# Kernel optimization log

Measured on AMD Instinct MI355X. Metric: run time of the kernel, lower is better.

Reference implementation:

```python
import jax, jax.numpy as jnp
import numpy as np

N = 100000          # nodes
E = 3200000         # edges
C_IN = 64
HIDDEN = 64
NUM_CLASSES = 10
NUM_GRAPHS = 256
EPS = 1e-5


def _graph_conv(x, src, dst, w_rel, w_root, b):
    # PyG GraphConv(aggr='mean'): out_i = W_rel * mean_{j->i} x_j + W_root * x_i + b
    msg_sum = jax.ops.segment_sum(x[src], dst, num_segments=N)            # [N, C]
    cnt = jax.ops.segment_sum(jnp.ones((src.shape[0], 1), x.dtype), dst,
                              num_segments=N)                             # [N, 1]
    agg = msg_sum / jnp.maximum(cnt, 1.0)
    return agg @ w_rel + x @ w_root + b


def _batch_norm(x, gamma, beta):
    # PyG BatchNorm in training mode: batch stats over the node dimension
    mean = jnp.mean(x, axis=0)
    var = jnp.var(x, axis=0)
    return (x - mean) * jax.lax.rsqrt(var + EPS) * gamma + beta


def setup_inputs() -> dict:
    key = jax.random.key(0)
    ks = jax.random.split(key, 20)
    x = jax.random.normal(ks[0], (N, C_IN), dtype=jnp.float32)
    edge_index = jax.random.randint(ks[1], (2, E), 0, N, dtype=jnp.int32)
    batch = jnp.sort(jax.random.randint(ks[2], (N,), 0, NUM_GRAPHS, dtype=jnp.int32))

    def lin(k, fan_in, fan_out):
        s = 1.0 / np.sqrt(fan_in)
        return jax.random.uniform(k, (fan_in, fan_out), jnp.float32, -s, s)

    dims = [(C_IN, 16), (16, 32), (32, 32), (32, HIDDEN)]
    params = {}
    ki = 3
    for i, (ci, co) in enumerate(dims, start=1):
        params[f"w_rel{i}"] = lin(ks[ki], ci, co); ki += 1
        params[f"w_root{i}"] = lin(ks[ki], ci, co); ki += 1
        params[f"b{i}"] = jnp.zeros((co,), jnp.float32)
        params[f"g{i}"] = jnp.ones((co,), jnp.float32)
        params[f"be{i}"] = jnp.zeros((co,), jnp.float32)
    params["w_lin1"] = lin(ks[ki], HIDDEN, HIDDEN); ki += 1
    params["b_lin1"] = jnp.zeros((HIDDEN,), jnp.float32)
    params["w_lin2"] = lin(ks[ki], HIDDEN, NUM_CLASSES); ki += 1
    params["b_lin2"] = jnp.zeros((NUM_CLASSES,), jnp.float32)

    return {"x": x, "edge_index": edge_index, "batch": batch, **params}


def reference(x, edge_index, batch,
              w_rel1, w_root1, b1, g1, be1,
              w_rel2, w_root2, b2, g2, be2,
              w_rel3, w_root3, b3, g3, be3,
              w_rel4, w_root4, b4, g4, be4,
              w_lin1, b_lin1, w_lin2, b_lin2):
    src, dst = edge_index[0], edge_index[1]
    h = jax.nn.elu(_batch_norm(_graph_conv(x, src, dst, w_rel1, w_root1, b1), g1, be1))
    h = jax.nn.elu(_batch_norm(_graph_conv(h, src, dst, w_rel2, w_root2, b2), g2, be2))
    h = jax.nn.elu(_batch_norm(_graph_conv(h, src, dst, w_rel3, w_root3, b3), g3, be3))
    h = jax.nn.elu(_batch_norm(_graph_conv(h, src, dst, w_rel4, w_root4, b4), g4, be4))
    # global mean pool over graphs
    pooled = jax.ops.segment_sum(h, batch, num_segments=NUM_GRAPHS)
    cnt = jax.ops.segment_sum(jnp.ones((N, 1), h.dtype), batch, num_segments=NUM_GRAPHS)
    pooled = pooled / jnp.maximum(cnt, 1.0)
    z = jax.nn.relu(pooled @ w_lin1 + b_lin1)
    # dropout omitted (deterministic / eval mode)
    logits = z @ w_lin2 + b_lin2
    return jax.nn.log_softmax(logits, axis=-1)
```

## Files before the change

kernel.cpp:

```cpp
#include <hip/hip_runtime.h>
#include <hip/hip_bf16.h>
#include <math.h>

#define NGRAPHS 256
#define BSHIFT 8
#define NBUCK 512
#define NSORT 256
#define LGRID 1024
#define GCHUNK 1024
#define SMASK 0x00FFFFFFu

__device__ __forceinline__ float bf2f(unsigned short u) {
    return __uint_as_float((unsigned)u << 16);
}
__device__ __forceinline__ unsigned short f2bf(float f) {
    unsigned u = __float_as_uint(f);
    unsigned r = (u + 0x7FFFu + ((u >> 16) & 1u)) >> 16;
    return (unsigned short)r;
}

__global__ __launch_bounds__(256) void k_bhist(const int* __restrict__ dst, int* __restrict__ hmat, int E,
                                               const float* __restrict__ x, const float* __restrict__ w_rel1,
                                               unsigned short* __restrict__ y1b,
                                               int* __restrict__ colpos, int N) {
    int bid = blockIdx.x, tid = threadIdx.x;
    if (bid < NSORT) {
        __shared__ int hist[NBUCK];
        for (int i = tid; i < NBUCK; i += 256) hist[i] = 0;
        __syncthreads();
        int chunk = (E + NSORT - 1) / NSORT;
        int lo = bid * chunk;
        int hi = lo + chunk; if (hi > E) hi = E;
        for (int i = lo + tid; i < hi; i += 256)
            atomicAdd(&hist[__builtin_nontemporal_load(dst + i) >> BSHIFT], 1);
        __syncthreads();
        for (int i = tid; i < NBUCK; i += 256) {
            int h = hist[i];
            int base = atomicAdd(&colpos[i], h);
            hmat[(size_t)bid * NBUCK + i] = base;
        }
    } else {
        __shared__ float s_rel[64 * 16];
        for (int i = tid; i < 64 * 16; i += 256) s_rel[i] = w_rel1[i];
        __syncthreads();
        int total = N * 4;
        int nb = gridDim.x - NSORT;
        for (int i = (bid - NSORT) * 256 + tid; i < total; i += nb * 256) {
            int n = i >> 2, c0 = (i & 3) << 2;
            const float4* mp = (const float4*)(x + (size_t)n * 64);
            float4 acc; acc.x = 0.f; acc.y = 0.f; acc.z = 0.f; acc.w = 0.f;
#pragma unroll
            for (int k2 = 0; k2 < 16; k2++) {
                float4 v = mp[k2];
                const float* wr = &s_rel[(k2 * 4) * 16 + c0];
                float4 w0 = *(const float4*)(wr);
                float4 w1 = *(const float4*)(wr + 16);
                float4 w2 = *(const float4*)(wr + 32);
                float4 w3 = *(const float4*)(wr + 48);
                acc.x += v.x * w0.x + v.y * w1.x + v.z * w2.x + v.w * w3.x;
                acc.y += v.x * w0.y + v.y * w1.y + v.z * w2.y + v.w * w3.y;
                acc.z += v.x * w0.z + v.y * w1.z + v.z * w2.z + v.w * w3.z;
                acc.w += v.x * w0.w + v.y * w1.w + v.z * w2.w + v.w * w3.w;
            }
            ushort4 o; o.x = f2bf(acc.x); o.y = f2bf(acc.y); o.z = f2bf(acc.z); o.w = f2bf(acc.w);
            *(ushort4*)(y1b + (size_t)n * 16 + c0) = o;
        }
    }
}

__global__ __launch_bounds__(512) void k_bscatter(const int* __restrict__ src, const int* __restrict__ dst,
                                                  const int* __restrict__ hmat, const int* __restrict__ colpos,
                                                  int* __restrict__ bstart_g,
                                                  unsigned* __restrict__ ebuf, int E) {
    __shared__ int s[NBUCK];
    __shared__ int cur[NBUCK];
    int tid = threadIdx.x;
    int b = blockIdx.x;
    int v = colpos[tid];
    s[tid] = v;
    __syncthreads();
    for (int off = 1; off < NBUCK; off <<= 1) {
        int t = (tid >= off) ? s[tid - off] : 0;
        __syncthreads();
        s[tid] += t;
        __syncthreads();
    }
    int excl = s[tid] - v;
    if (b == 0) {
        bstart_g[tid] = excl;
        if (tid == NBUCK - 1) bstart_g[NBUCK] = s[NBUCK - 1];
    }
    cur[tid] = excl + hmat[(size_t)b * NBUCK + tid];
    __syncthreads();
    int chunk = (E + NSORT - 1) / NSORT;
    int lo = b * chunk;
    int hi = lo + chunk; if (hi > E) hi = E;
    for (int i = lo + tid; i < hi; i += 512) {
        int d = __builtin_nontemporal_load(dst + i);
        int sv = __builtin_nontemporal_load(src + i);
        int p = atomicAdd(&cur[d >> BSHIFT], 1);
        ebuf[p] = (unsigned)sv | ((unsigned)(d & 255) << 24);
    }
}

__global__ __launch_bounds__(256) void k_sort2(const unsigned* __restrict__ ebuf, const int* __restrict__ bstart,
                                               int* __restrict__ csr, int* __restrict__ row_start, int N) {
    __shared__ int hist[256];
    __shared__ int sc[256];
    __shared__ int scur[256];
    int b = blockIdx.x;
    int e0 = bstart[b], e1 = bstart[b + 1];
    hist[threadIdx.x] = 0;
    __syncthreads();
    for (int i = e0 + threadIdx.x; i < e1; i += 256)
        atomicAdd(&hist[__builtin_nontemporal_load(ebuf + i) >> 24], 1);
    __syncthreads();
    sc[threadIdx.x] = hist[threadIdx.x];
    __syncthreads();
    for (int off = 1; off < 256; off <<= 1) {
        int t = (threadIdx.x >= off) ? sc[threadIdx.x - off] : 0;
        __syncthreads();
        sc[threadIdx.x] += t;
        __syncthreads();
    }
    {
        int inc = sc[threadIdx.x];
        int ex = inc - hist[threadIdx.x];
        scur[threadIdx.x] = e0 + ex;
        int node = (b << BSHIFT) + threadIdx.x;
        if (node < N) row_start[node] = e0 + ex;
        if (node == N - 1) row_start[N] = e0 + inc;
    }
    __syncthreads();
    for (int i = e0 + threadIdx.x; i < e1; i += 256) {
        unsigned w = __builtin_nontemporal_load(ebuf + i);
        int p = atomicAdd(&scur[w >> 24], 1);
        csr[p] = (int)(w & SMASK);
    }
}

template <int C>
__global__ __launch_bounds__(256) void k_gather(const unsigned short* __restrict__ h,
                                                const int* __restrict__ row_start,
                                                const int* __restrict__ csr, float* __restrict__ agg, int N) {
    constexpr int LPR = C / 4;
    constexpr int EPP = 64 / LPR;
    constexpr int BATCH = 4 * EPP;
    __shared__ int sbuf[GCHUNK];
    int lane = threadIdx.x & 63;
    int w = threadIdx.x >> 6;
    int nb = blockIdx.x * 4;
    int wid = nb + w;
    bool act = wid < N;
    int nb_end = nb + 4; if (nb_end > N) nb_end = N;
    int eb0 = row_start[nb];
    int eb1 = row_start[nb_end];
    int r0 = act ? row_start[wid] : 0;
    int r1 = act ? row_start[wid + 1] : 0;
    int es = lane / LPR;
    int cq = (lane % LPR) * 4;

    float a0 = 0.f, a1 = 0.f, a2 = 0.f, a3 = 0.f;
    for (int base = eb0; base < eb1; base += GCHUNK) {
        int len = eb1 - base; if (len > GCHUNK) len = GCHUNK;
        __syncthreads();
        for (int i = threadIdx.x; i < len; i += 256)
            sbuf[i] = __builtin_nontemporal_load(csr + base + i);
        __syncthreads();
        if (act) {
            int lo = (r0 > base ? r0 : base) - base;
            int hiv = r1 < base + len ? r1 : base + len;
            int hi = hiv - base;
            for (int j0 = lo; j0 < hi; j0 += BATCH) {
                int s[4]; bool p[4];
#pragma unroll
                for (int u = 0; u < 4; u++) {
                    int j = j0 + u * EPP + es;
                    p[u] = j < hi;
                    s[u] = sbuf[p[u] ? j : j0];
                }
                ushort4 v[4];
#pragma unroll
                for (int u = 0; u < 4; u++)
                    v[u] = *(const ushort4*)(h + (size_t)s[u] * C + cq);
#pragma unroll
                for (int u = 0; u < 4; u++) {
                    if (p[u]) {
                        a0 += bf2f(v[u].x); a1 += bf2f(v[u].y);
                        a2 += bf2f(v[u].z); a3 += bf2f(v[u].w);
                    }
                }
            }
        }
    }
#pragma unroll
    for (int off = LPR; off < 64; off <<= 1) {
        a0 += __shfl_xor(a0, off, 64);
        a1 += __shfl_xor(a1, off, 64);
        a2 += __shfl_xor(a2, off, 64);
        a3 += __shfl_xor(a3, off, 64);
    }
    if (act && lane < LPR) {
        int deg = r1 - r0;
        float rec = 1.0f / (float)(deg > 0 ? deg : 1);
        float4 o; o.x = a0 * rec; o.y = a1 * rec; o.z = a2 * rec; o.w = a3 * rec;
        *(float4*)(agg + (size_t)wid * C + cq) = o;
    }
}

template <int CI, int CO, bool HAS_REL, bool ADD_AGG, bool IN_BF16>
__global__ __launch_bounds__(256) void k_lin_stats(const void* __restrict__ hroot_v, const float* __restrict__ hrel,
                                                   const float* __restrict__ w_rel, const float* __restrict__ w_root,
                                                   const float* __restrict__ bias,
                                                   float* __restrict__ out, float* __restrict__ gsl, int N) {
    constexpr int NPW = 64 / CO;
    __shared__ float part[4][2 * CO];
    int tid = threadIdx.x;
    int lane = tid & 63;
    int w = tid >> 6;
    int ch = lane % CO;
    int sub = lane / CO;

    float wro[CI];
#pragma unroll
    for (int ci = 0; ci < CI; ci++) wro[ci] = w_root[ci * CO + ch];
    float wre[HAS_REL ? CI : 1];
    if (HAS_REL) {
#pragma unroll
        for (int ci = 0; ci < CI; ci++) wre[ci] = w_rel[ci * CO + ch];
    }
    float bch = bias[ch];

    int ngrp = (N + NPW - 1) / NPW;
    int gw = blockIdx.x * 4 + w;
    int nwv = gridDim.x * 4;
    float ssum = 0.f, qsum = 0.f;
    for (int g = gw; g < ngrp; g += nwv) {
        int n = g * NPW + sub;
        if (n < N) {
            float acc = bch;
            if (ADD_AGG) acc += hrel[(size_t)n * CO + ch];
#pragma unroll
            for (int cb = 0; cb < CI / 4; cb++) {
                float f0, f1, f2, f3;
                if (IN_BF16) {
                    ushort4 v = *(const ushort4*)((const unsigned short*)hroot_v + (size_t)n * CI + cb * 4);
                    f0 = bf2f(v.x); f1 = bf2f(v.y); f2 = bf2f(v.z); f3 = bf2f(v.w);
                } else {
                    float4 v = *(const float4*)((const float*)hroot_v + (size_t)n * CI + cb * 4);
                    f0 = v.x; f1 = v.y; f2 = v.z; f3 = v.w;
                }
                acc += f0 * wro[cb * 4 + 0] + f1 * wro[cb * 4 + 1]
                     + f2 * wro[cb * 4 + 2] + f3 * wro[cb * 4 + 3];
                if (HAS_REL) {
                    float4 a = *(const float4*)(hrel + (size_t)n * CI + cb * 4);
                    acc += a.x * wre[cb * 4 + 0] + a.y * wre[cb * 4 + 1]
                         + a.z * wre[cb * 4 + 2] + a.w * wre[cb * 4 + 3];
                }
            }
            out[(size_t)n * CO + ch] = acc;
            ssum += acc; qsum += acc * acc;
        }
    }
#pragma unroll
    for (int off = CO; off < 64; off <<= 1) {
        ssum += __shfl_xor(ssum, off, 64);
        qsum += __shfl_xor(qsum, off, 64);
    }
    if (lane < CO) { part[w][lane] = ssum; part[w][CO + lane] = qsum; }
    __syncthreads();
    if (tid < 2 * CO) {
        float v = part[0][tid] + part[1][tid] + part[2][tid] + part[3][tid];
        atomicAdd(&gsl[tid], v);
    }
}

template <int CO>
__global__ __launch_bounds__(256) void k_bn_elu(const float* __restrict__ h, const float* __restrict__ gsl,
                                                const float* __restrict__ g, const float* __restrict__ be,
                                                unsigned short* __restrict__ hb, float invN, int N) {
    __shared__ float sc[CO], sh[CO];
    if (threadIdx.x < CO) {
        int c = threadIdx.x;
        float mean = gsl[c] * invN;
        float var = gsl[CO + c] * invN - mean * mean;
        float s = g[c] * rsqrtf(var + 1e-5f);
        sc[c] = s;
        sh[c] = be[c] - mean * s;
    }
    __syncthreads();
    int total = N * (CO / 4);
    int i = blockIdx.x * 256 + threadIdx.x;
    if (i >= total) return;
    float4 v = ((const float4*)h)[i];
    int cq = (i % (CO / 4)) * 4;
    v.x = v.x * sc[cq + 0] + sh[cq + 0];
    v.y = v.y * sc[cq + 1] + sh[cq + 1];
    v.z = v.z * sc[cq + 2] + sh[cq + 2];
    v.w = v.w * sc[cq + 3] + sh[cq + 3];
    v.x = v.x > 0.f ? v.x : expm1f(v.x);
    v.y = v.y > 0.f ? v.y : expm1f(v.y);
    v.z = v.z > 0.f ? v.z : expm1f(v.z);
    v.w = v.w > 0.f ? v.w : expm1f(v.w);
    ushort4 o;
    o.x = f2bf(v.x); o.y = f2bf(v.y); o.z = f2bf(v.z); o.w = f2bf(v.w);
    ((ushort4*)hb)[i] = o;
}

__global__ __launch_bounds__(256) void k_bn_elu_pool(const float* __restrict__ h, const float* __restrict__ gsl,
                                                     const float* __restrict__ g, const float* __restrict__ be,
                                                     const int* __restrict__ batch,
                                                     float* __restrict__ pooled, float* __restrict__ cntg,
                                                     float invN, int N) {
    __shared__ float sc[64], sh[64];
    if (threadIdx.x < 64) {
        int c = threadIdx.x;
        float mean = gsl[c] * invN;
        float var = gsl[64 + c] * invN - mean * mean;
        float s = g[c] * rsqrtf(var + 1e-5f);
        sc[c] = s;
        sh[c] = be[c] - mean * s;
    }
    __syncthreads();
    int lane = threadIdx.x & 63;
    int wid = blockIdx.x * 4 + (threadIdx.x >> 6);
    int n0 = wid * 16;
    if (n0 >= N) return;
    float scl = sc[lane];
    float shl = sh[lane];
    int nmax = N - n0; if (nmax > 16) nmax = 16;
    int cur = batch[n0];
    float acc = 0.f;
    float run = 0.f;
    for (int k = 0; k < nmax; k++) {
        int gg = batch[n0 + k];
        if (gg != cur) {
            atomicAdd(&pooled[(size_t)cur * 64 + lane], acc);
            if (lane == 0) atomicAdd(&cntg[cur], run);
            cur = gg; acc = 0.f; run = 0.f;
        }
        float v = h[(size_t)(n0 + k) * 64 + lane] * scl + shl;
        v = v > 0.f ? v : expm1f(v);
        acc += v;
        run += 1.f;
    }
    atomicAdd(&pooled[(size_t)cur * 64 + lane], acc);
    if (lane == 0) atomicAdd(&cntg[cur], run);
}

__global__ __launch_bounds__(256) void k_head(const float* __restrict__ pooled, const float* __restrict__ cntg,
                                              const float* __restrict__ w1, const float* __restrict__ b1,
                                              const float* __restrict__ w2, const float* __restrict__ b2,
                                              float* __restrict__ out) {
    int g = threadIdx.x;
    float rec = 1.0f / fmaxf(cntg[g], 1.0f);
    float p[64];
    {
        const float4* pp = (const float4*)(pooled + (size_t)g * 64);
#pragma unroll
        for (int i = 0; i < 16; i++) {
            float4 v = pp[i];
            p[4 * i + 0] = v.x * rec; p[4 * i + 1] = v.y * rec;
            p[4 * i + 2] = v.z * rec; p[4 * i + 3] = v.w * rec;
        }
    }
    float lg[10];
#pragma unroll
    for (int t = 0; t < 10; t++) lg[t] = b2[t];
#pragma unroll 1
    for (int j = 0; j < 64; j++) {
        float a = b1[j];
#pragma unroll
        for (int k = 0; k < 64; k++) a += p[k] * w1[k * 64 + j];
        a = fmaxf(a, 0.f);
#pragma unroll
        for (int t = 0; t < 10; t++) lg[t] += a * w2[j * 10 + t];
    }
    float m = -1e30f;
#pragma unroll
    for (int t = 0; t < 10; t++) m = fmaxf(m, lg[t]);
    float s = 0.f;
#pragma unroll
    for (int t = 0; t < 10; t++) s += expf(lg[t] - m);
    float lse = m + logf(s);
#pragma unroll
    for (int t = 0; t < 10; t++) out[(size_t)g * 10 + t] = lg[t] - lse;
}

extern "C" void kernel_launch(void* const* d_in, const int* in_sizes, int n_in,
                              void* d_out, int out_size, void* d_ws, size_t ws_size,
                              hipStream_t stream) {
    const float* x = (const float*)d_in[0];
    const int* ei = (const int*)d_in[1];
    const int* batch = (const int*)d_in[2];
    const int N = in_sizes[0] / 64;
    const int E = in_sizes[1] / 2;
    const int* src = ei;
    const int* dst = ei + E;

    const float* w_rel1 = (const float*)d_in[3];
    const float* w_root1 = (const float*)d_in[4];
    const float* b1 = (const float*)d_in[5];
    const float* g1 = (const float*)d_in[6];
    const float* be1 = (const float*)d_in[7];
    const float* w_rel2 = (const float*)d_in[8];
    const float* w_root2 = (const float*)d_in[9];
    const float* b2 = (const float*)d_in[10];
    const float* g2 = (const float*)d_in[11];
    const float* be2 = (const float*)d_in[12];
    const float* w_rel3 = (const float*)d_in[13];
    const float* w_root3 = (const float*)d_in[14];
    const float* b3 = (const float*)d_in[15];
    const float* g3 = (const float*)d_in[16];
    const float* be3 = (const float*)d_in[17];
    const float* w_rel4 = (const float*)d_in[18];
    const float* w_root4 = (const float*)d_in[19];
    const float* b4 = (const float*)d_in[20];
    const float* g4 = (const float*)d_in[21];
    const float* be4 = (const float*)d_in[22];
    const float* w_lin1 = (const float*)d_in[23];
    const float* b_lin1 = (const float*)d_in[24];
    const float* w_lin2 = (const float*)d_in[25];
    const float* b_lin2 = (const float*)d_in[26];

    char* ws = (char*)d_ws;
    size_t off = 0;
    auto alloc = [&](size_t bytes) { size_t o = off; off += (bytes + 255) & ~(size_t)255; return o; };
    int* hmat = (int*)(ws + alloc((size_t)NSORT * NBUCK * 4));
    int* bstart = (int*)(ws + alloc((size_t)(NBUCK + 1) * 4));
    unsigned* ebuf = (unsigned*)(ws + alloc((size_t)E * 4));
    int* csr = (int*)(ws + alloc((size_t)E * 4));
    int* row_start = (int*)(ws + alloc((size_t)(N + 1) * 4));
    float* agg = (float*)(ws + alloc((size_t)N * 32 * 4));
    unsigned short* y1b = (unsigned short*)(ws + alloc((size_t)N * 16 * 2));
    unsigned short* hb = (unsigned short*)(ws + alloc((size_t)N * 64 * 2));
    float* bufA = (float*)(ws + alloc((size_t)N * 64 * 4));
    const int zwords = NBUCK + 512 + NGRAPHS * 64 + NGRAPHS;
    int* colpos = (int*)(ws + alloc((size_t)zwords * 4));
    float* gs = (float*)(colpos + NBUCK);
    float* pooled = gs + 512;
    float* cntg = pooled + NGRAPHS * 64;

    hipMemsetAsync(colpos, 0, (size_t)zwords * 4, stream);

    const float invN = 1.0f / (float)N;
    const int gbl = (N + 3) / 4;

    k_bhist<<<1024, 256, 0, stream>>>(dst, hmat, E, x, w_rel1, y1b, colpos, N);
    k_bscatter<<<NSORT, 512, 0, stream>>>(src, dst, hmat, colpos, bstart, ebuf, E);
    k_sort2<<<NBUCK, 256, 0, stream>>>(ebuf, bstart, csr, row_start, N);

    k_gather<16><<<gbl, 256, 0, stream>>>(y1b, row_start, csr, agg, N);
    k_lin_stats<64, 16, false, true, false><<<LGRID, 256, 0, stream>>>(
        x, agg, nullptr, w_root1, b1, bufA, gs + 0, N);
    k_bn_elu<16><<<(N * 4 + 255) / 256, 256, 0, stream>>>(bufA, gs + 0, g1, be1, hb, invN, N);

    k_gather<16><<<gbl, 256, 0, stream>>>(hb, row_start, csr, agg, N);
    k_lin_stats<16, 32, true, false, true><<<LGRID, 256, 0, stream>>>(
        hb, agg, w_rel2, w_root2, b2, bufA, gs + 128, N);
    k_bn_elu<32><<<(N * 8 + 255) / 256, 256, 0, stream>>>(bufA, gs + 128, g2, be2, hb, invN, N);

    k_gather<32><<<gbl, 256, 0, stream>>>(hb, row_start, csr, agg, N);
    k_lin_stats<32, 32, true, false, true><<<LGRID, 256, 0, stream>>>(
        hb, agg, w_rel3, w_root3, b3, bufA, gs + 256, N);
    k_bn_elu<32><<<(N * 8 + 255) / 256, 256, 0, stream>>>(bufA, gs + 256, g3, be3, hb, invN, N);

    k_gather<32><<<gbl, 256, 0, stream>>>(hb, row_start, csr, agg, N);
    k_lin_stats<32, 64, true, false, true><<<LGRID, 256, 0, stream>>>(
        hb, agg, w_rel4, w_root4, b4, bufA, gs + 384, N);
    int waves16 = (N + 15) / 16;
    k_bn_elu_pool<<<(waves16 + 3) / 4, 256, 0, stream>>>(
        bufA, gs + 384, g4, be4, batch, pooled, cntg, invN, N);

    k_head<<<1, 256, 0, stream>>>(pooled, cntg, w_lin1, b_lin1, w_lin2, b_lin2, (float*)d_out);
}
```

Before: 616.4 us.

## Fuse neighbor gather with linear transform and BN stats per layer

Merges the CSR mean-gather kernel and the linear+batch-stat kernel into one persistent grid-stride kernel per layer. Each wave aggregates one node's neighbors, then applies W_rel and W_root through wave shuffles and writes the output and partial sums directly. This removes the fp32 agg round trip through global memory and one launch per layer. In exchange, weights are read from global inside the loop instead of being held in registers, and the matvec is serialized through shuffles, which may add per-node latency.

```diff
diff --git a/kernel.cpp b/kernel.cpp
--- a/kernel.cpp
+++ b/kernel.cpp
@@ -6,7 +6,7 @@
 #define BSHIFT 8
 #define NBUCK 512
 #define NSORT 256
-#define LGRID 1024
+#define FGRID 2048
 #define GCHUNK 1024
 #define SMASK 0x00FFFFFFu
 
@@ -139,133 +139,117 @@
     }
 }
 
-template <int C>
-__global__ __launch_bounds__(256) void k_gather(const unsigned short* __restrict__ h,
-                                                const int* __restrict__ row_start,
-                                                const int* __restrict__ csr, float* __restrict__ agg, int N) {
-    constexpr int LPR = C / 4;
+template <int CI, int CIR, int CO, bool HAS_REL, bool ROOT_F32>
+__global__ __launch_bounds__(256) void k_gconv_stats(const unsigned short* __restrict__ hsrc,
+                                                     const void* __restrict__ hroot_v,
+                                                     const int* __restrict__ row_start, const int* __restrict__ csr,
+                                                     const float* __restrict__ w_rel, const float* __restrict__ w_root,
+                                                     const float* __restrict__ bias,
+                                                     float* __restrict__ out, float* __restrict__ gsl, int N) {
+    constexpr int LPR = CI / 4;
     constexpr int EPP = 64 / LPR;
     constexpr int BATCH = 4 * EPP;
     __shared__ int sbuf[GCHUNK];
-    int lane = threadIdx.x & 63;
-    int w = threadIdx.x >> 6;
-    int nb = blockIdx.x * 4;
-    int wid = nb + w;
-    bool act = wid < N;
-    int nb_end = nb + 4; if (nb_end > N) nb_end = N;
-    int eb0 = row_start[nb];
-    int eb1 = row_start[nb_end];
-    int r0 = act ? row_start[wid] : 0;
-    int r1 = act ? row_start[wid + 1] : 0;
-    int es = lane / LPR;
-    int cq = (lane % LPR) * 4;
-
-    float a0 = 0.f, a1 = 0.f, a2 = 0.f, a3 = 0.f;
-    for (int base = eb0; base < eb1; base += GCHUNK) {
-        int len = eb1 - base; if (len > GCHUNK) len = GCHUNK;
-        __syncthreads();
-        for (int i = threadIdx.x; i < len; i += 256)
-            sbuf[i] = __builtin_nontemporal_load(csr + base + i);
-        __syncthreads();
-        if (act) {
-            int lo = (r0 > base ? r0 : base) - base;
-            int hiv = r1 < base + len ? r1 : base + len;
-            int hi = hiv - base;
-            for (int j0 = lo; j0 < hi; j0 += BATCH) {
-                int s[4]; bool p[4];
-#pragma unroll
-                for (int u = 0; u < 4; u++) {
-                    int j = j0 + u * EPP + es;
-                    p[u] = j < hi;
-                    s[u] = sbuf[p[u] ? j : j0];
-                }
-                ushort4 v[4];
-#pragma unroll
-                for (int u = 0; u < 4; u++)
-                    v[u] = *(const ushort4*)(h + (size_t)s[u] * C + cq);
-#pragma unroll
-                for (int u = 0; u < 4; u++) {
-                    if (p[u]) {
-                        a0 += bf2f(v[u].x); a1 += bf2f(v[u].y);
-                        a2 += bf2f(v[u].z); a3 += bf2f(v[u].w);
-                    }
-                }
-            }
-        }
-    }
-#pragma unroll
-    for (int off = LPR; off < 64; off <<= 1) {
-        a0 += __shfl_xor(a0, off, 64);
-        a1 += __shfl_xor(a1, off, 64);
-        a2 += __shfl_xor(a2, off, 64);
-        a3 += __shfl_xor(a3, off, 64);
-    }
-    if (act && lane < LPR) {
-        int deg = r1 - r0;
-        float rec = 1.0f / (float)(deg > 0 ? deg : 1);
-        float4 o; o.x = a0 * rec; o.y = a1 * rec; o.z = a2 * rec; o.w = a3 * rec;
-        *(float4*)(agg + (size_t)wid * C + cq) = o;
-    }
-}
-
-template <int CI, int CO, bool HAS_REL, bool ADD_AGG, bool IN_BF16>
-__global__ __launch_bounds__(256) void k_lin_stats(const void* __restrict__ hroot_v, const float* __restrict__ hrel,
-                                                   const float* __restrict__ w_rel, const float* __restrict__ w_root,
-                                                   const float* __restrict__ bias,
-                                                   float* __restrict__ out, float* __restrict__ gsl, int N) {
-    constexpr int NPW = 64 / CO;
     __shared__ float part[4][2 * CO];
     int tid = threadIdx.x;
     int lane = tid & 63;
     int w = tid >> 6;
-    int ch = lane % CO;
-    int sub = lane / CO;
-
-    float wro[CI];
-#pragma unroll
-    for (int ci = 0; ci < CI; ci++) wro[ci] = w_root[ci * CO + ch];
-    float wre[HAS_REL ? CI : 1];
-    if (HAS_REL) {
-#pragma unroll
-        for (int ci = 0; ci < CI; ci++) wre[ci] = w_rel[ci * CO + ch];
-    }
-    float bch = bias[ch];
-
-    int ngrp = (N + NPW - 1) / NPW;
-    int gw = blockIdx.x * 4 + w;
-    int nwv = gridDim.x * 4;
+    int es = lane / LPR;
+    int cq = (lane % LPR) * 4;
+    int c = lane;
     float ssum = 0.f, qsum = 0.f;
-    for (int g = gw; g < ngrp; g += nwv) {
-        int n = g * NPW + sub;
-        if (n < N) {
-            float acc = bch;
-            if (ADD_AGG) acc += hrel[(size_t)n * CO + ch];
-#pragma unroll
-            for (int cb = 0; cb < CI / 4; cb++) {
-                float f0, f1, f2, f3;
-                if (IN_BF16) {
-                    ushort4 v = *(const ushort4*)((const unsigned short*)hroot_v + (size_t)n * CI + cb * 4);
-                    f0 = bf2f(v.x); f1 = bf2f(v.y); f2 = bf2f(v.z); f3 = bf2f(v.w);
-                } else {
-                    float4 v = *(const float4*)((const float*)hroot_v + (size_t)n * CI + cb * 4);
-                    f0 = v.x; f1 = v.y; f2 = v.z; f3 = v.w;
-                }
-                acc += f0 * wro[cb * 4 + 0] + f1 * wro[cb * 4 + 1]
-                     + f2 * wro[cb * 4 + 2] + f3 * wro[cb * 4 + 3];
-                if (HAS_REL) {
-                    float4 a = *(const float4*)(hrel + (size_t)n * CI + cb * 4);
-                    acc += a.x * wre[cb * 4 + 0] + a.y * wre[cb * 4 + 1]
-                         + a.z * wre[cb * 4 + 2] + a.w * wre[cb * 4 + 3];
+
+    int ngrp = (N + 3) >> 2;
+    for (int grp = blockIdx.x; grp < ngrp; grp += gridDim.x) {
+        int nb = grp * 4;
+        int wid = nb + w;
+        bool act = wid < N;
+        int nb_end = nb + 4; if (nb_end > N) nb_end = N;
+        int eb0 = row_start[nb];
+        int eb1 = row_start[nb_end];
+        int r0 = act ? row_start[wid] : 0;
+        int r1 = act ? row_start[wid + 1] : 0;
+
+        float a0 = 0.f, a1 = 0.f, a2 = 0.f, a3 = 0.f;
+        for (int base = eb0; base < eb1; base += GCHUNK) {
+            int len = eb1 - base; if (len > GCHUNK) len = GCHUNK;
+            __syncthreads();
+            for (int i = tid; i < len; i += 256)
+                sbuf[i] = __builtin_nontemporal_load(csr + base + i);
+            __syncthreads();
+            if (act) {
+                int lo = (r0 > base ? r0 : base) - base;
+                int hiv = r1 < base + len ? r1 : base + len;
+                int hi = hiv - base;
+                for (int j0 = lo; j0 < hi; j0 += BATCH) {
+                    int s[4]; bool p[4];
+#pragma unroll
+                    for (int u = 0; u < 4; u++) {
+                        int j = j0 + u * EPP + es;
+                        p[u] = j < hi;
+                        s[u] = sbuf[p[u] ? j : j0];
+                    }
+                    ushort4 v[4];
+#pragma unroll
+                    for (int u = 0; u < 4; u++)
+                        v[u] = *(const ushort4*)(hsrc + (size_t)s[u] * CI + cq);
+#pragma unroll
+                    for (int u = 0; u < 4; u++) {
+                        if (p[u]) {
+                            a0 += bf2f(v[u].x); a1 += bf2f(v[u].y);
+                            a2 += bf2f(v[u].z); a3 += bf2f(v[u].w);
+                        }
+                    }
                 }
             }
-            out[(size_t)n * CO + ch] = acc;
-            ssum += acc; qsum += acc * acc;
-        }
-    }
-#pragma unroll
-    for (int off = CO; off < 64; off <<= 1) {
-        ssum += __shfl_xor(ssum, off, 64);
-        qsum += __shfl_xor(qsum, off, 64);
+        }
+        if (act) {
+#pragma unroll
+            for (int off = LPR; off < 64; off <<= 1) {
+                a0 += __shfl_xor(a0, off, 64);
+                a1 += __shfl_xor(a1, off, 64);
+                a2 += __shfl_xor(a2, off, 64);
+                a3 += __shfl_xor(a3, off, 64);
+            }
+            int deg = r1 - r0;
+            float rec = 1.0f / (float)(deg > 0 ? deg : 1);
+            a0 *= rec; a1 *= rec; a2 *= rec; a3 *= rec;
+            float aa[4] = {a0, a1, a2, a3};
+
+            float rr[4];
+            if (ROOT_F32) {
+                const float4* xp = (const float4*)((const float*)hroot_v + (size_t)wid * CIR);
+                float4 v = xp[lane % (CIR / 4)];
+                rr[0] = v.x; rr[1] = v.y; rr[2] = v.z; rr[3] = v.w;
+            } else {
+                const unsigned short* hp = (const unsigned short*)hroot_v;
+                ushort4 v = *(const ushort4*)(hp + (size_t)wid * CIR + (size_t)(lane % (CIR / 4)) * 4);
+                rr[0] = bf2f(v.x); rr[1] = bf2f(v.y); rr[2] = bf2f(v.z); rr[3] = bf2f(v.w);
+            }
+
+            if (c < CO) {
+                float acc = bias[c];
+#pragma unroll
+                for (int ci = 0; ci < CIR; ci++) {
+                    float hv = __shfl(rr[ci & 3], ci >> 2, 64);
+                    acc += hv * w_root[ci * CO + c];
+                }
+                if (HAS_REL) {
+#pragma unroll
+                    for (int ci = 0; ci < CI; ci++) {
+                        float av = __shfl(aa[ci & 3], ci >> 2, 64);
+                        acc += av * w_rel[ci * CO + c];
+                    }
+                } else {
+                    float t0 = __shfl(a0, c >> 2, 64), t1 = __shfl(a1, c >> 2, 64);
+                    float t2 = __shfl(a2, c >> 2, 64), t3 = __shfl(a3, c >> 2, 64);
+                    float av = (c & 2) ? ((c & 1) ? t3 : t2) : ((c & 1) ? t1 : t0);
+                    acc += av;
+                }
+                out[(size_t)wid * CO + c] = acc;
+                ssum += acc; qsum += acc * acc;
+            }
+        }
     }
     if (lane < CO) { part[w][lane] = ssum; part[w][CO + lane] = qsum; }
     __syncthreads();
@@ -431,7 +415,6 @@
     unsigned* ebuf = (unsigned*)(ws + alloc((size_t)E * 4));
     int* csr = (int*)(ws + alloc((size_t)E * 4));
     int* row_start = (int*)(ws + alloc((size_t)(N + 1) * 4));
-    float* agg = (float*)(ws + alloc((size_t)N * 32 * 4));
     unsigned short* y1b = (unsigned short*)(ws + alloc((size_t)N * 16 * 2));
     unsigned short* hb = (unsigned short*)(ws + alloc((size_t)N * 64 * 2));
     float* bufA = (float*)(ws + alloc((size_t)N * 64 * 4));
@@ -444,30 +427,25 @@
     hipMemsetAsync(colpos, 0, (size_t)zwords * 4, stream);
 
     const float invN = 1.0f / (float)N;
-    const int gbl = (N + 3) / 4;
 
     k_bhist<<<1024, 256, 0, stream>>>(dst, hmat, E, x, w_rel1, y1b, colpos, N);
     k_bscatter<<<NSORT, 512, 0, stream>>>(src, dst, hmat, colpos, bstart, ebuf, E);
     k_sort2<<<NBUCK, 256, 0, stream>>>(ebuf, bstart, csr, row_start, N);
 
-    k_gather<16><<<gbl, 256, 0, stream>>>(y1b, row_start, csr, agg, N);
-    k_lin_stats<64, 16, false, true, false><<<LGRID, 256, 0, stream>>>(
-        x, agg, nullptr, w_root1, b1, bufA, gs + 0, N);
+    k_gconv_stats<16, 64, 16, false, true><<<FGRID, 256, 0, stream>>>(
+        y1b, x, row_start, csr, nullptr, w_root1, b1, bufA, gs + 0, N);
     k_bn_elu<16><<<(N * 4 + 255) / 256, 256, 0, stream>>>(bufA, gs + 0, g1, be1, hb, invN, N);
 
-    k_gather<16><<<gbl, 256, 0, stream>>>(hb, row_start, csr, agg, N);
-    k_lin_stats<16, 32, true, false, true><<<LGRID, 256, 0, stream>>>(
-        hb, agg, w_rel2, w_root2, b2, bufA, gs + 128, N);
+    k_gconv_stats<16, 16, 32, true, false><<<FGRID, 256, 0, stream>>>(
+        hb, hb, row_start, csr, w_rel2, w_root2, b2, bufA, gs + 128, N);
     k_bn_elu<32><<<(N * 8 + 255) / 256, 256, 0, stream>>>(bufA, gs + 128, g2, be2, hb, invN, N);
 
-    k_gather<32><<<gbl, 256, 0, stream>>>(hb, row_start, csr, agg, N);
-    k_lin_stats<32, 32, true, false, true><<<LGRID, 256, 0, stream>>>(
-        hb, agg, w_rel3, w_root3, b3, bufA, gs + 256, N);
+    k_gconv_stats<32, 32, 32, true, false><<<FGRID, 256, 0, stream>>>(
+        hb, hb, row_start, csr, w_rel3, w_root3, b3, bufA, gs + 256, N);
     k_bn_elu<32><<<(N * 8 + 255) / 256, 256, 0, stream>>>(bufA, gs + 256, g3, be3, hb, invN, N);
 
-    k_gather<32><<<gbl, 256, 0, stream>>>(hb, row_start, csr, agg, N);
-    k_lin_stats<32, 64, true, false, true><<<LGRID, 256, 0, stream>>>(
-        hb, agg, w_rel4, w_root4, b4, bufA, gs + 384, N);
+    k_gconv_stats<32, 32, 64, true, false><<<FGRID, 256, 0, stream>>>(
+        hb, hb, row_start, csr, w_rel4, w_root4, b4, bufA, gs + 384, N);
     int waves16 = (N + 15) / 16;
     k_bn_elu_pool<<<(waves16 + 3) / 4, 256, 0, stream>>>(
         bufA, gs + 384, g4, be4, batch, pooled, cntg, invN, N);
```

New measurement: 916.9 us. 48.7% more time.
